# Optimization experiments

Hardware: AMD Instinct MI355X
Metric: run time of the kernel (lower is better)

The kernel has to match this reference:

```python
import jax, jax.numpy as jnp
import numpy as np

N_NODES = 50000
N_EDGES = 800000
HIDDEN = 64


def _init_linear(key, fan_in, fan_out):
    kw, kb = jax.random.split(key)
    lim = 1.0 / np.sqrt(fan_in)
    W = jax.random.uniform(kw, (fan_in, fan_out), jnp.float32, -lim, lim)
    b = jax.random.uniform(kb, (fan_out,), jnp.float32, -lim, lim)
    return W, b


def setup_inputs() -> dict:
    key = jax.random.key(0)
    ks = jax.random.split(key, 10)
    feat = jax.random.normal(ks[0], (N_NODES, HIDDEN), jnp.float32)
    x = jax.random.normal(ks[1], (N_NODES, 3), jnp.float32)
    src = jax.random.randint(ks[2], (N_EDGES,), 0, N_NODES, jnp.int32)
    dst = jax.random.randint(ks[3], (N_EDGES,), 0, N_NODES, jnp.int32)
    # message MLP: (2H+1) -> H -> H, relu after both layers (last_activation=mid)
    W1, b1 = _init_linear(ks[4], 2 * HIDDEN + 1, HIDDEN)
    W2, b2 = _init_linear(ks[5], HIDDEN, HIDDEN)
    # soft edge gate: H -> 1
    we, be = _init_linear(ks[6], HIDDEN, 1)
    # update MLP: H -> H -> H, relu mid, no last activation
    U1, c1 = _init_linear(ks[7], HIDDEN, HIDDEN)
    U2, c2 = _init_linear(ks[8], HIDDEN, HIDDEN)
    return dict(feat=feat, x=x, src=src, dst=dst,
                W1=W1, b1=b1, W2=W2, b2=b2, we=we, be=be,
                U1=U1, c1=c1, U2=U2, c2=c2)


def reference(feat, x, src, dst, W1, b1, W2, b2, we, be, U1, c1, U2, c2):
    # per-edge squared distance between endpoint coordinates: [E, 1]
    sqd = jnp.sum((x[src] - x[dst]) ** 2, axis=-1, keepdims=True)
    # message input: [E, 2H+1]
    msg_in = jnp.concatenate([feat[src], feat[dst], sqd], axis=-1)
    # 2-layer message MLP with relu mid and last activation
    m = jax.nn.relu(jax.nn.relu(msg_in @ W1 + b1) @ W2 + b2)
    # sigmoid soft-edge gate: [E, 1]
    gate = jax.nn.sigmoid(m @ we + be)
    # scatter-sum gated messages to destination nodes: [N, H]
    m_sum = jax.ops.segment_sum(m * gate, dst, num_segments=N_NODES)
    # node update MLP on (m_sum + feat), residual add
    h = m_sum + feat
    h_new = jax.nn.relu(h @ U1 + c1) @ U2 + c2
    return h_new + feat
```

## Files before the change

### kernel.cpp

```cpp
#include <hip/hip_runtime.h>
#include <hip/hip_bf16.h>
#include <stdint.h>

#define N_NODES 50000
#define N_EDGES 800000
#define HDIM 64
#define SCAN_N (N_NODES + 1)

#define MSUM_OFF   0
#define EP_OFF     12800000
#define DEG_OFF    (EP_OFF + 12800000)
#define OFFS_OFF   (DEG_OFF + 204800)
#define POS_OFF    (OFFS_OFF + 204800)
#define FB_OFF     (POS_OFF + 204800)
#define W1T_OFF    (FB_OFF + (size_t)N_NODES * HDIM * 2)
#define W2T_OFF    (W1T_OFF + 16384)
#define U1T_OFF    (W2T_OFF + 8192)
#define U2T_OFF    (U1T_OFF + 8192)
#define WS_NEED    (U2T_OFF + 8192)

#define CVT_BLOCKS   1563
#define PREPW_BLOCKS 80
#define MZ_BLOCKS    3125
#define HIST_BLOCKS  1024

typedef __attribute__((ext_vector_type(8))) short short8;
typedef __attribute__((ext_vector_type(4))) float floatx4;

__device__ __forceinline__ float bf2f(unsigned short u) {
    union { unsigned int i; float f; } v; v.i = ((unsigned int)u) << 16; return v.f;
}
__device__ __forceinline__ unsigned short f2bf(float f) {
    __hip_bfloat16 h = __float2bfloat16(f);
    return *reinterpret_cast<unsigned short*>(&h);
}

__device__ __forceinline__ int detect_is_bf16(const unsigned short* p) {
    int cnt = 0;
    #pragma unroll
    for (int i = 0; i < 64; ++i) {
        unsigned short b = p[i];
        int e = (b >> 7) & 0xFF;
        cnt += ((e >= 97 && e <= 157) || (b & 0x7FFF) == 0) ? 1 : 0;
    }
    return cnt >= 56;
}

__device__ __forceinline__ float getf(const void* p, unsigned int i, int isb) {
    return isb ? bf2f(((const unsigned short*)p)[i]) : ((const float*)p)[i];
}

__device__ __forceinline__ short8 get8bf(const void* p, unsigned int i, int isb) {
    if (isb) {
        return *reinterpret_cast<const short8*>((const short*)p + i);
    } else {
        const float4 f0 = *reinterpret_cast<const float4*>((const float*)p + i);
        const float4 f1 = *reinterpret_cast<const float4*>((const float*)p + i + 4);
        short8 a;
        a[0] = (short)f2bf(f0.x); a[1] = (short)f2bf(f0.y);
        a[2] = (short)f2bf(f0.z); a[3] = (short)f2bf(f0.w);
        a[4] = (short)f2bf(f1.x); a[5] = (short)f2bf(f1.y);
        a[6] = (short)f2bf(f1.z); a[7] = (short)f2bf(f1.w);
        return a;
    }
}

#define COMPILER_FENCE() asm volatile("" ::: "memory")
#define WAIT_LDS() __builtin_amdgcn_s_waitcnt(0xC07F)

__global__ __launch_bounds__(256) void prep_kernel(
    const void* __restrict__ feat, unsigned short* __restrict__ fb,
    const void* __restrict__ W1, const void* __restrict__ W2,
    const void* __restrict__ U1, const void* __restrict__ U2,
    unsigned short* __restrict__ w1t, unsigned short* __restrict__ w2t,
    unsigned short* __restrict__ u1t, unsigned short* __restrict__ u2t,
    const int* __restrict__ dst, int* __restrict__ deg,
    uint4* __restrict__ msumz)
{
    const int b = blockIdx.x;
    if (b < CVT_BLOCKS) {
        const int isb = detect_is_bf16((const unsigned short*)feat);
        int i = (b * 256 + threadIdx.x) * 8;
        if (i >= N_NODES * HDIM) return;
        if (isb) {
            *reinterpret_cast<uint4*>(fb + i) =
                *reinterpret_cast<const uint4*>((const unsigned short*)feat + i);
        } else {
            float4 f0 = *reinterpret_cast<const float4*>((const float*)feat + i);
            float4 f1 = *reinterpret_cast<const float4*>((const float*)feat + i + 4);
            ushort4 a = {f2bf(f0.x), f2bf(f0.y), f2bf(f0.z), f2bf(f0.w)};
            ushort4 c = {f2bf(f1.x), f2bf(f1.y), f2bf(f1.z), f2bf(f1.w)};
            *reinterpret_cast<ushort4*>(fb + i)     = a;
            *reinterpret_cast<ushort4*>(fb + i + 4) = c;
        }
    } else if (b < CVT_BLOCKS + PREPW_BLOCKS) {
        const int isb = detect_is_bf16((const unsigned short*)feat);
        int idx = (b - CVT_BLOCKS) * 256 + threadIdx.x;
        if (idx < 8192) {
            int n = idx >> 7, k = idx & 127;
            w1t[idx] = f2bf(getf(W1, k * 64 + n, isb));
        } else if (idx < 12288) {
            int i = idx - 8192, n = i >> 6, k = i & 63;
            w2t[i] = f2bf(getf(W2, k * 64 + n, isb));
        } else if (idx < 16384) {
            int i = idx - 12288, n = i >> 6, k = i & 63;
            u1t[i] = f2bf(getf(U1, k * 64 + n, isb));
        } else if (idx < 20480) {
            int i = idx - 16384, n = i >> 6, k = i & 63;
            u2t[i] = f2bf(getf(U2, k * 64 + n, isb));
        }
    } else if (b < CVT_BLOCKS + PREPW_BLOCKS + MZ_BLOCKS) {
        int i = (b - CVT_BLOCKS - PREPW_BLOCKS) * 256 + threadIdx.x;
        if (i < N_NODES * HDIM / 4)
            msumz[i] = (uint4){0u, 0u, 0u, 0u};
    } else {
        int e0 = (b - CVT_BLOCKS - PREPW_BLOCKS - MZ_BLOCKS) * 256 + threadIdx.x;
        for (int e = e0; e < N_EDGES; e += HIST_BLOCKS * 256)
            atomicAdd(&deg[dst[e]], 1);
    }
}

__global__ void scan1_kernel(const int* __restrict__ deg, int* __restrict__ part) {
    __shared__ int s[1024];
    int g = blockIdx.x * 1024 + threadIdx.x;
    s[threadIdx.x] = (g < SCAN_N) ? deg[g] : 0;
    __syncthreads();
    for (int off = 512; off > 0; off >>= 1) {
        if (threadIdx.x < off) s[threadIdx.x] += s[threadIdx.x + off];
        __syncthreads();
    }
    if (threadIdx.x == 0) part[blockIdx.x] = s[0];
}

__global__ void scan2_kernel(int* __restrict__ part, int nparts) {
    if (threadIdx.x == 0) {
        int run = 0;
        for (int i = 0; i < nparts; ++i) { int t = part[i]; part[i] = run; run += t; }
    }
}

__global__ void scan3_kernel(const int* __restrict__ deg, const int* __restrict__ part,
                             int* __restrict__ offs, int* __restrict__ pos) {
    __shared__ int s[1024];
    int g = blockIdx.x * 1024 + threadIdx.x;
    int v = (g < SCAN_N) ? deg[g] : 0;
    s[threadIdx.x] = v;
    __syncthreads();
    for (int off = 1; off < 1024; off <<= 1) {
        int t = (threadIdx.x >= off) ? s[threadIdx.x - off] : 0;
        __syncthreads();
        s[threadIdx.x] += t;
        __syncthreads();
    }
    int excl = s[threadIdx.x] - v + part[blockIdx.x];
    if (g < SCAN_N) { offs[g] = excl; pos[g] = excl; }
}

__global__ __launch_bounds__(256) void permute_kernel(
    const void* __restrict__ feat, const void* __restrict__ xpos,
    const int* __restrict__ src, const int* __restrict__ dst,
    int* __restrict__ pos, uint4* __restrict__ epack)
{
    const int isb = detect_is_bf16((const unsigned short*)feat);
    int e = blockIdx.x * 256 + threadIdx.x;
    if (e < N_EDGES) {
        int s = src[e], d = dst[e];
        int slot = atomicAdd(&pos[d], 1);
        float dx = getf(xpos, s * 3 + 0, isb) - getf(xpos, d * 3 + 0, isb);
        float dy = getf(xpos, s * 3 + 1, isb) - getf(xpos, d * 3 + 1, isb);
        float dz = getf(xpos, s * 3 + 2, isb) - getf(xpos, d * 3 + 2, isb);
        float sqd = dx * dx + dy * dy + dz * dz;
        uint4 p;
        p.x = (unsigned int)s;
        p.y = (unsigned int)d;
        p.z = __float_as_uint(sqd);
        p.w = 0u;
        epack[slot] = p;
    }
}

template <bool CSR>
__global__ __launch_bounds__(256, 2) void edge_kernel(
    const unsigned short* __restrict__ fbf,
    const unsigned short* __restrict__ w1t, const unsigned short* __restrict__ w2t,
    const void* __restrict__ feat, const void* __restrict__ xpos,
    const int* __restrict__ src, const int* __restrict__ dst,
    const uint4* __restrict__ epack,
    const void* __restrict__ W1, const void* __restrict__ b1,
    const void* __restrict__ W2, const void* __restrict__ b2,
    const void* __restrict__ we, const void* __restrict__ be,
    float* __restrict__ msum, unsigned int msum_cap)
{
    __shared__ __align__(16) short sW1[16][64][8];
    __shared__ __align__(16) short sW2[8][64][8];
    __shared__ __align__(16) short sA2[4][16][72];
    __shared__ int sD[4][16];

    const int isb  = detect_is_bf16((const unsigned short*)feat);
    const int tid  = threadIdx.x;
    const int wave = tid >> 6;
    const int lane = tid & 63;
    const int l15  = lane & 15;
    const int quad = lane >> 4;

    short8 bw1[4][4];
    short8 bw2[2][4];
    if (CSR) {
        for (int i = tid; i < 16 * 64; i += 256) {
            int f = i >> 6, l = i & 63;
            int n = (f & 3) * 16 + (l & 15);
            int k0 = (f >> 2) * 32 + (l >> 4) * 8;
            *reinterpret_cast<short8*>(&sW1[f][l][0]) =
                *reinterpret_cast<const short8*>(w1t + n * 128 + k0);
        }
        for (int i = tid; i < 8 * 64; i += 256) {
            int f = i >> 6, l = i & 63;
            int n = (f & 3) * 16 + (l & 15);
            int k0 = (f >> 2) * 32 + (l >> 4) * 8;
            *reinterpret_cast<short8*>(&sW2[f][l][0]) =
                *reinterpret_cast<const short8*>(w2t + n * 64 + k0);
        }
        __syncthreads();
    } else {
        #pragma unroll
        for (int c = 0; c < 4; ++c)
            #pragma unroll
            for (int nt = 0; nt < 4; ++nt) {
                short8 b;
                #pragma unroll
                for (int j = 0; j < 8; ++j)
                    b[j] = (short)f2bf(getf(W1, (c * 32 + quad * 8 + j) * 64 + nt * 16 + l15, isb));
                bw1[c][nt] = b;
            }
        #pragma unroll
        for (int c = 0; c < 2; ++c)
            #pragma unroll
            for (int nt = 0; nt < 4; ++nt) {
                short8 b;
                #pragma unroll
                for (int j = 0; j < 8; ++j)
                    b[j] = (short)f2bf(getf(W2, (c * 32 + quad * 8 + j) * 64 + nt * 16 + l15, isb));
                bw2[c][nt] = b;
            }
    }

    float b1r[4], w1lr[4], b2r[4], wer[4];
    #pragma unroll
    for (int nt = 0; nt < 4; ++nt) {
        int n = nt * 16 + l15;
        b1r[nt]  = getf(b1, n, isb);
        w1lr[nt] = getf(W1, 128 * 64 + n, isb);
        b2r[nt]  = getf(b2, n, isb);
        wer[nt]  = getf(we, n, isb);
    }
    const float ber = getf(be, 0, isb);
    const int rowb = quad * 4;

    const int ntiles = N_EDGES / 64;
    for (int t = blockIdx.x; t < ntiles; t += gridDim.x) {
        const int ebase = t * 64 + wave * 16;

        int sidx = 0, didx = 0;
        float sqd = 0.f;
        if (CSR) {
            if (lane < 16) {
                uint4 p = epack[ebase + lane];
                sidx = (int)p.x;
                didx = (int)p.y;
                sqd  = __uint_as_float(p.z);
                sD[wave][lane] = didx;
            }
        } else {
            if (lane < 16) {
                int e = ebase + lane;
                sidx = src[e];
                didx = dst[e];
                float dx = getf(xpos, sidx * 3 + 0, isb) - getf(xpos, didx * 3 + 0, isb);
                float dy = getf(xpos, sidx * 3 + 1, isb) - getf(xpos, didx * 3 + 1, isb);
                float dz = getf(xpos, sidx * 3 + 2, isb) - getf(xpos, didx * 3 + 2, isb);
                sqd = dx * dx + dy * dy + dz * dz;
            }
        }
        const int sn     = __shfl(sidx, l15);
        const int dn_row = __shfl(didx, l15);

        floatx4 acc[4];
        #pragma unroll
        for (int nt = 0; nt < 4; ++nt) acc[nt] = (floatx4){0.f, 0.f, 0.f, 0.f};
        #pragma unroll
        for (int c = 0; c < 4; ++c) {
            const int node = (c < 2) ? sn : dn_row;
            const unsigned int aoff = (unsigned int)node * 64u + (c & 1) * 32 + quad * 8;
            short8 a;
            if (CSR) a = *reinterpret_cast<const short8*>((const short*)fbf + aoff);
            else     a = get8bf(feat, aoff, isb);
            #pragma unroll
            for (int nt = 0; nt < 4; ++nt) {
                short8 b;
                if (CSR) b = *reinterpret_cast<const short8*>(&sW1[c * 4 + nt][lane][0]);
                else     b = bw1[c][nt];
                acc[nt] = __builtin_amdgcn_mfma_f32_16x16x32_bf16(a, b, acc[nt], 0, 0, 0);
            }
        }

        float sq[4];
        #pragma unroll
        for (int r = 0; r < 4; ++r) sq[r] = __shfl(sqd, rowb + r);
        #pragma unroll
        for (int nt = 0; nt < 4; ++nt)
            #pragma unroll
            for (int r = 0; r < 4; ++r) {
                float v = fmaxf(acc[nt][r] + b1r[nt] + sq[r] * w1lr[nt], 0.f);
                sA2[wave][rowb + r][nt * 16 + l15] = (short)f2bf(v);
            }
        COMPILER_FENCE();
        WAIT_LDS();

        floatx4 acc2[4];
        #pragma unroll
        for (int nt = 0; nt < 4; ++nt) acc2[nt] = (floatx4){0.f, 0.f, 0.f, 0.f};
        #pragma unroll
        for (int c = 0; c < 2; ++c) {
            short8 a = *reinterpret_cast<const short8*>(&sA2[wave][l15][c * 32 + quad * 8]);
            #pragma unroll
            for (int nt = 0; nt < 4; ++nt) {
                short8 b;
                if (CSR) b = *reinterpret_cast<const short8*>(&sW2[c * 4 + nt][lane][0]);
                else     b = bw2[c][nt];
                acc2[nt] = __builtin_amdgcn_mfma_f32_16x16x32_bf16(a, b, acc2[nt], 0, 0, 0);
            }
        }
        COMPILER_FENCE();

        float mval[4][4];
        float part[4] = {0.f, 0.f, 0.f, 0.f};
        #pragma unroll
        for (int nt = 0; nt < 4; ++nt)
            #pragma unroll
            for (int r = 0; r < 4; ++r) {
                float v = fmaxf(acc2[nt][r] + b2r[nt], 0.f);
                mval[nt][r] = v;
                part[r] += v * wer[nt];
            }
        #pragma unroll
        for (int off = 1; off < 16; off <<= 1)
            #pragma unroll
            for (int r = 0; r < 4; ++r) part[r] += __shfl_xor(part[r], off);
        float gate[4];
        #pragma unroll
        for (int r = 0; r < 4; ++r)
            gate[r] = 1.f / (1.f + __expf(-(part[r] + ber)));

        if (CSR) {
            #pragma unroll
            for (int nt = 0; nt < 4; ++nt)
                #pragma unroll
                for (int r = 0; r < 4; ++r)
                    sA2[wave][rowb + r][nt * 16 + l15] = (short)f2bf(mval[nt][r] * gate[r]);
            COMPILER_FENCE();
            WAIT_LDS();
            float run = 0.f;
            int dcur = sD[wave][0];
            #pragma unroll
            for (int r = 0; r < 16; ++r) {
                run += bf2f((unsigned short)sA2[wave][r][lane]);
                int dnxt = (r < 15) ? sD[wave][r + 1] : -1;
                if (dnxt != dcur) {
                    unsafeAtomicAdd(&msum[(unsigned int)dcur * 64u + lane], run);
                    run = 0.f;
                    dcur = dnxt;
                }
            }
            COMPILER_FENCE();
        } else {
            #pragma unroll
            for (int r = 0; r < 4; ++r) {
                int dn = __shfl(didx, rowb + r);
                unsigned int base = (unsigned int)dn * 64u;
                if (base + 64u <= msum_cap) {
                    #pragma unroll
                    for (int nt = 0; nt < 4; ++nt)
                        unsafeAtomicAdd(&msum[base + nt * 16 + l15], mval[nt][r] * gate[r]);
                }
            }
        }
    }
}

__global__ __launch_bounds__(256, 2) void node_kernel(
    const float* __restrict__ msum,
    const unsigned short* __restrict__ u1t, const unsigned short* __restrict__ u2t,
    const void* __restrict__ feat,
    const void* __restrict__ U1, const void* __restrict__ c1v,
    const void* __restrict__ U2, const void* __restrict__ c2v,
    void* __restrict__ out)
{
    __shared__ __align__(16) short sT[4][16][72];
    __shared__ __align__(16) float sF[4][16][68];

    const int isb  = detect_is_bf16((const unsigned short*)feat);
    const int tid  = threadIdx.x;
    const int wave = tid >> 6;
    const int lane = tid & 63;
    const int l15  = lane & 15;
    const int quad = lane >> 4;

    short8 u1f[2][4], u2f[2][4];
    if (u1t) {
        #pragma unroll
        for (int nt = 0; nt < 4; ++nt) {
            const int n = nt * 16 + l15;
            #pragma unroll
            for (int c = 0; c < 2; ++c) {
                u1f[c][nt] = *reinterpret_cast<const short8*>(u1t + n * 64 + c * 32 + quad * 8);
                u2f[c][nt] = *reinterpret_cast<const short8*>(u2t + n * 64 + c * 32 + quad * 8);
            }
        }
    } else {
        #pragma unroll
        for (int c = 0; c < 2; ++c)
            #pragma unroll
            for (int nt = 0; nt < 4; ++nt) {
                short8 a, b;
                #pragma unroll
                for (int j = 0; j < 8; ++j) {
                    int k = c * 32 + quad * 8 + j, n = nt * 16 + l15;
                    a[j] = (short)f2bf(getf(U1, k * 64 + n, isb));
                    b[j] = (short)f2bf(getf(U2, k * 64 + n, isb));
                }
                u1f[c][nt] = a; u2f[c][nt] = b;
            }
    }
    float c1r[4], c2r[4];
    #pragma unroll
    for (int nt = 0; nt < 4; ++nt) {
        c1r[nt] = getf(c1v, nt * 16 + l15, isb);
        c2r[nt] = getf(c2v, nt * 16 + l15, isb);
    }
    const int rowb = quad * 4;

    const int ntile = (N_NODES + 15) / 16;
    const int t = blockIdx.x * 4 + wave;
    if (t < ntile) {
        const int node = t * 16 + l15;

        short8 ah[2];
        #pragma unroll
        for (int c = 0; c < 2; ++c) {
            unsigned int off = (unsigned int)node * 64u + c * 32 + quad * 8;
            float4 m0 = *reinterpret_cast<const float4*>(msum + off);
            float4 m1 = *reinterpret_cast<const float4*>(msum + off + 4);
            float mv[8] = {m0.x, m0.y, m0.z, m0.w, m1.x, m1.y, m1.z, m1.w};
            float hv[8];
            if (isb) {
                short8 fv = *reinterpret_cast<const short8*>((const short*)feat + off);
                #pragma unroll
                for (int j = 0; j < 8; ++j) hv[j] = bf2f((unsigned short)fv[j]);
            } else {
                float4 f0 = *reinterpret_cast<const float4*>((const float*)feat + off);
                float4 f1 = *reinterpret_cast<const float4*>((const float*)feat + off + 4);
                hv[0] = f0.x; hv[1] = f0.y; hv[2] = f0.z; hv[3] = f0.w;
                hv[4] = f1.x; hv[5] = f1.y; hv[6] = f1.z; hv[7] = f1.w;
            }
            short8 a;
            #pragma unroll
            for (int j = 0; j < 8; ++j) a[j] = (short)f2bf(mv[j] + hv[j]);
            ah[c] = a;
        }

        floatx4 acc[4];
        #pragma unroll
        for (int nt = 0; nt < 4; ++nt) acc[nt] = (floatx4){0.f, 0.f, 0.f, 0.f};
        #pragma unroll
        for (int c = 0; c < 2; ++c)
            #pragma unroll
            for (int nt = 0; nt < 4; ++nt)
                acc[nt] = __builtin_amdgcn_mfma_f32_16x16x32_bf16(ah[c], u1f[c][nt], acc[nt], 0, 0, 0);

        #pragma unroll
        for (int nt = 0; nt < 4; ++nt)
            #pragma unroll
            for (int r = 0; r < 4; ++r) {
                float v = fmaxf(acc[nt][r] + c1r[nt], 0.f);
                sT[wave][rowb + r][nt * 16 + l15] = (short)f2bf(v);
            }
        COMPILER_FENCE();
        WAIT_LDS();

        floatx4 acc2[4];
        #pragma unroll
        for (int nt = 0; nt < 4; ++nt) acc2[nt] = (floatx4){0.f, 0.f, 0.f, 0.f};
        #pragma unroll
        for (int c = 0; c < 2; ++c) {
            short8 a = *reinterpret_cast<const short8*>(&sT[wave][l15][c * 32 + quad * 8]);
            #pragma unroll
            for (int nt = 0; nt < 4; ++nt)
                acc2[nt] = __builtin_amdgcn_mfma_f32_16x16x32_bf16(a, u2f[c][nt], acc2[nt], 0, 0, 0);
        }
        COMPILER_FENCE();

        #pragma unroll
        for (int nt = 0; nt < 4; ++nt)
            #pragma unroll
            for (int r = 0; r < 4; ++r)
                sF[wave][rowb + r][nt * 16 + l15] = acc2[nt][r] + c2r[nt];
        COMPILER_FENCE();
        WAIT_LDS();

        const unsigned int ob = (unsigned int)node * 64u + quad * 16;
        if (isb) {
            const unsigned short* fp = (const unsigned short*)feat + ob;
            unsigned short* op = (unsigned short*)out + ob;
            #pragma unroll
            for (int k = 0; k < 2; ++k) {
                ushort4 o0, o1;
                float4 v0 = *reinterpret_cast<const float4*>(&sF[wave][l15][quad * 16 + k * 8]);
                float4 v1 = *reinterpret_cast<const float4*>(&sF[wave][l15][quad * 16 + k * 8 + 4]);
                const ushort4 f0 = *reinterpret_cast<const ushort4*>(fp + k * 8);
                const ushort4 f1 = *reinterpret_cast<const ushort4*>(fp + k * 8 + 4);
                o0.x = f2bf(v0.x + bf2f(f0.x)); o0.y = f2bf(v0.y + bf2f(f0.y));
                o0.z = f2bf(v0.z + bf2f(f0.z)); o0.w = f2bf(v0.w + bf2f(f0.w));
                o1.x = f2bf(v1.x + bf2f(f1.x)); o1.y = f2bf(v1.y + bf2f(f1.y));
                o1.z = f2bf(v1.z + bf2f(f1.z)); o1.w = f2bf(v1.w + bf2f(f1.w));
                *reinterpret_cast<ushort4*>(op + k * 8)     = o0;
                *reinterpret_cast<ushort4*>(op + k * 8 + 4) = o1;
            }
        } else {
            const float* fp = (const float*)feat + ob;
            float* op = (float*)out + ob;
            #pragma unroll
            for (int k = 0; k < 4; ++k) {
                float4 v = *reinterpret_cast<const float4*>(&sF[wave][l15][quad * 16 + k * 4]);
                float4 f = *reinterpret_cast<const float4*>(fp + k * 4);
                float4 o = {v.x + f.x, v.y + f.y, v.z + f.z, v.w + f.w};
                *reinterpret_cast<float4*>(op + k * 4) = o;
            }
        }
        COMPILER_FENCE();
    }
}

extern "C" void kernel_launch(void* const* d_in, const int* in_sizes, int n_in,
                              void* d_out, int out_size, void* d_ws, size_t ws_size,
                              hipStream_t stream) {
    const void* feat = d_in[0];
    const void* x    = d_in[1];
    const int* src   = (const int*)d_in[2];
    const int* dst   = (const int*)d_in[3];
    const void* W1   = d_in[4];
    const void* b1   = d_in[5];
    const void* W2   = d_in[6];
    const void* b2   = d_in[7];
    const void* we   = d_in[8];
    const void* be   = d_in[9];
    const void* U1   = d_in[10];
    const void* c1   = d_in[11];
    const void* U2   = d_in[12];
    const void* c2   = d_in[13];
    char* ws = (char*)d_ws;

    if (ws_size >= WS_NEED) {
        float* msum = (float*)(ws + MSUM_OFF);
        uint4* epack = (uint4*)(ws + EP_OFF);
        int* deg  = (int*)(ws + DEG_OFF);
        int* offs = (int*)(ws + OFFS_OFF);
        int* pos  = (int*)(ws + POS_OFF);
        unsigned short* fb  = (unsigned short*)(ws + FB_OFF);
        unsigned short* w1t = (unsigned short*)(ws + W1T_OFF);
        unsigned short* w2t = (unsigned short*)(ws + W2T_OFF);
        unsigned short* u1t = (unsigned short*)(ws + U1T_OFF);
        unsigned short* u2t = (unsigned short*)(ws + U2T_OFF);

        hipMemsetAsync(deg, 0, 204800, stream);
        prep_kernel<<<CVT_BLOCKS + PREPW_BLOCKS + MZ_BLOCKS + HIST_BLOCKS, 256, 0, stream>>>(
            feat, fb, W1, W2, U1, U2, w1t, w2t, u1t, u2t, dst, deg, (uint4*)msum);
        scan1_kernel<<<49, 1024, 0, stream>>>(deg, offs + 51200 - 64);
        scan2_kernel<<<1, 64, 0, stream>>>(offs + 51200 - 64, 49);
        scan3_kernel<<<49, 1024, 0, stream>>>(deg, offs + 51200 - 64, offs, pos);
        permute_kernel<<<(N_EDGES + 255) / 256, 256, 0, stream>>>(feat, x, src, dst, pos, epack);
        edge_kernel<true><<<2500, 256, 0, stream>>>(fb, w1t, w2t, feat, x, src, dst, epack,
                                                    W1, b1, W2, b2, we, be,
                                                    msum, (unsigned int)(N_NODES * HDIM));
        node_kernel<<<((N_NODES + 15) / 16 + 3) / 4, 256, 0, stream>>>(
            msum, u1t, u2t, feat, U1, c1, U2, c2, d_out);
    } else {
        float* msum = (float*)ws;
        size_t need = (size_t)N_NODES * HDIM * sizeof(float);
        size_t clr  = need < ws_size ? need : ws_size;
        unsigned int cap = (unsigned int)(ws_size / sizeof(float));
        if (cap > (unsigned int)(N_NODES * HDIM)) cap = (unsigned int)(N_NODES * HDIM);

        hipMemsetAsync(msum, 0, clr, stream);
        edge_kernel<false><<<2500, 256, 0, stream>>>(nullptr, nullptr, nullptr, feat, x, src, dst,
                                                     nullptr, W1, b1, W2, b2, we, be,
                                                     msum, cap);
        node_kernel<<<((N_NODES + 15) / 16 + 3) / 4, 256, 0, stream>>>(
            msum, nullptr, nullptr, feat, U1, c1, U2, c2, d_out);
    }
}
```

Baseline: 273.1 us.

## Segment-reduce edge messages in registers via ballot and widen edge blocks to 512

```diff
diff --git a/kernel.cpp b/kernel.cpp
--- a/kernel.cpp
+++ b/kernel.cpp
@@ -180,7 +180,7 @@
 }
 
 template <bool CSR>
-__global__ __launch_bounds__(256, 2) void edge_kernel(
+__global__ __launch_bounds__(512, 6) void edge_kernel(
     const unsigned short* __restrict__ fbf,
     const unsigned short* __restrict__ w1t, const unsigned short* __restrict__ w2t,
     const void* __restrict__ feat, const void* __restrict__ xpos,
@@ -193,8 +193,7 @@
 {
     __shared__ __align__(16) short sW1[16][64][8];
     __shared__ __align__(16) short sW2[8][64][8];
-    __shared__ __align__(16) short sA2[4][16][72];
-    __shared__ int sD[4][16];
+    __shared__ __align__(16) short sA2[8][16][72];
 
     const int isb  = detect_is_bf16((const unsigned short*)feat);
     const int tid  = threadIdx.x;
@@ -206,14 +205,14 @@
     short8 bw1[4][4];
     short8 bw2[2][4];
     if (CSR) {
-        for (int i = tid; i < 16 * 64; i += 256) {
+        for (int i = tid; i < 16 * 64; i += 512) {
             int f = i >> 6, l = i & 63;
             int n = (f & 3) * 16 + (l & 15);
             int k0 = (f >> 2) * 32 + (l >> 4) * 8;
             *reinterpret_cast<short8*>(&sW1[f][l][0]) =
                 *reinterpret_cast<const short8*>(w1t + n * 128 + k0);
         }
-        for (int i = tid; i < 8 * 64; i += 256) {
+        for (int i = tid; i < 8 * 64; i += 512) {
             int f = i >> 6, l = i & 63;
             int n = (f & 3) * 16 + (l & 15);
             int k0 = (f >> 2) * 32 + (l >> 4) * 8;
@@ -256,9 +255,9 @@
     const float ber = getf(be, 0, isb);
     const int rowb = quad * 4;
 
-    const int ntiles = N_EDGES / 64;
+    const int ntiles = N_EDGES / 128;
     for (int t = blockIdx.x; t < ntiles; t += gridDim.x) {
-        const int ebase = t * 64 + wave * 16;
+        const int ebase = t * 128 + wave * 16;
 
         int sidx = 0, didx = 0;
         float sqd = 0.f;
@@ -268,7 +267,6 @@
                 sidx = (int)p.x;
                 didx = (int)p.y;
                 sqd  = __uint_as_float(p.z);
-                sD[wave][lane] = didx;
             }
         } else {
             if (lane < 16) {
@@ -352,26 +350,33 @@
             gate[r] = 1.f / (1.f + __expf(-(part[r] + ber)));
 
         if (CSR) {
-            #pragma unroll
-            for (int nt = 0; nt < 4; ++nt)
+            int nd = __shfl(didx, (lane + 1) & 15);
+            int flag = (lane == 15) || (nd != didx);
+            unsigned long long bal = __ballot(lane < 16 && flag);
+            unsigned int m16 = (unsigned int)(bal & 0xFFFFull);
+            int lo = 0;
+            while (m16) {
+                int hi = __ffs(m16) - 1;
+                float s0 = 0.f, s1 = 0.f, s2 = 0.f, s3 = 0.f;
                 #pragma unroll
-                for (int r = 0; r < 4; ++r)
-                    sA2[wave][rowb + r][nt * 16 + l15] = (short)f2bf(mval[nt][r] * gate[r]);
-            COMPILER_FENCE();
-            WAIT_LDS();
-            float run = 0.f;
-            int dcur = sD[wave][0];
-            #pragma unroll
-            for (int r = 0; r < 16; ++r) {
-                run += bf2f((unsigned short)sA2[wave][r][lane]);
-                int dnxt = (r < 15) ? sD[wave][r + 1] : -1;
-                if (dnxt != dcur) {
-                    unsafeAtomicAdd(&msum[(unsigned int)dcur * 64u + lane], run);
-                    run = 0.f;
-                    dcur = dnxt;
+                for (int r = 0; r < 4; ++r) {
+                    int gr = rowb + r;
+                    float g = (gr >= lo && gr <= hi) ? gate[r] : 0.f;
+                    s0 += g * mval[0][r];
+                    s1 += g * mval[1][r];
+                    s2 += g * mval[2][r];
+                    s3 += g * mval[3][r];
                 }
-            }
-            COMPILER_FENCE();
+                s0 += __shfl_xor(s0, 16); s0 += __shfl_xor(s0, 32);
+                s1 += __shfl_xor(s1, 16); s1 += __shfl_xor(s1, 32);
+                s2 += __shfl_xor(s2, 16); s2 += __shfl_xor(s2, 32);
+                s3 += __shfl_xor(s3, 16); s3 += __shfl_xor(s3, 32);
+                int d = __shfl(didx, hi);
+                float v = (quad == 0) ? s0 : (quad == 1) ? s1 : (quad == 2) ? s2 : s3;
+                unsafeAtomicAdd(&msum[(unsigned int)d * 64u + (unsigned int)quad * 16u + l15], v);
+                lo = hi + 1;
+                m16 &= m16 - 1;
+            }
         } else {
             #pragma unroll
             for (int r = 0; r < 4; ++r) {
@@ -578,7 +583,7 @@
         scan2_kernel<<<1, 64, 0, stream>>>(offs + 51200 - 64, 49);
         scan3_kernel<<<49, 1024, 0, stream>>>(deg, offs + 51200 - 64, offs, pos);
         permute_kernel<<<(N_EDGES + 255) / 256, 256, 0, stream>>>(feat, x, src, dst, pos, epack);
-        edge_kernel<true><<<2500, 256, 0, stream>>>(fb, w1t, w2t, feat, x, src, dst, epack,
+        edge_kernel<true><<<1250, 512, 0, stream>>>(fb, w1t, w2t, feat, x, src, dst, epack,
                                                     W1, b1, W2, b2, we, be,
                                                     msum, (unsigned int)(N_NODES * HDIM));
         node_kernel<<<((N_NODES + 15) / 16 + 3) / 4, 256, 0, stream>>>(
@@ -591,7 +596,7 @@
         if (cap > (unsigned int)(N_NODES * HDIM)) cap = (unsigned int)(N_NODES * HDIM);
 
         hipMemsetAsync(msum, 0, clr, stream);
-        edge_kernel<false><<<2500, 256, 0, stream>>>(nullptr, nullptr, nullptr, feat, x, src, dst,
+        edge_kernel<false><<<1250, 512, 0, stream>>>(nullptr, nullptr, nullptr, feat, x, src, dst,
                                                      nullptr, W1, b1, W2, b2, we, be,
                                                      msum, cap);
         node_kernel<<<((N_NODES + 15) / 16 + 3) / 4, 256, 0, stream>>>(
```

After: 263.0 us. 3.7% less time.
